# Performance work log

Hardware: AMD Instinct MI355X
Metric: run time of the kernel (lower is better)

Reference implementation:

```python
import jax, jax.numpy as jnp
import numpy as np

TEMPERATURE = 0.07
MARGIN = 0.2
SHUF_ID_OFFSET = 100000


def _normalize(x):
    # matches F.normalize(x + 1e-8, dim=-1) with default eps=1e-12
    v = x + 1e-8
    n = jnp.linalg.norm(v, axis=-1, keepdims=True)
    return v / jnp.maximum(n, 1e-12)


def setup_inputs() -> dict:
    key = jax.random.key(0)
    k1, k2, k3, k4 = jax.random.split(key, 4)
    M, C, D = 1024, 3, 512
    return {
        "motion_embs": jax.random.normal(k1, (M, D), dtype=jnp.float32),
        "text_embs": jax.random.normal(k2, (M, C, D), dtype=jnp.float32),
        "shuffled_text_embs": jax.random.normal(k3, (M, C, D), dtype=jnp.float32),
        "motion_ids": jax.random.randint(k4, (M,), 0, 256, dtype=jnp.int64 if jax.config.jax_enable_x64 else jnp.int32),
    }


def reference(motion_embs, text_embs, shuffled_text_embs, motion_ids):
    M, C, D = text_embs.shape
    m = _normalize(motion_embs)                       # [M, D]
    t = _normalize(text_embs).reshape(M * C, D)       # [M*C, D]
    s = _normalize(shuffled_text_embs).reshape(M * C, D)

    emb = jnp.concatenate([m, t, s], axis=0)          # [N, D], N = M + 2*M*C
    ids = jnp.concatenate([
        motion_ids,
        jnp.repeat(motion_ids, C),
        jnp.repeat(motion_ids + SHUF_ID_OFFSET, C),
    ])

    sim = (emb @ emb.T) / TEMPERATURE                 # [N, N]
    N = emb.shape[0]
    same = ids[None, :] == ids[:, None]
    eye = jnp.eye(N, dtype=bool)
    pos_mask = same & ~eye
    neg_mask = (~same) & ~eye

    exp_sim = jnp.exp(sim)
    # denominator over positives + negatives (all off-diagonal), as in the original
    denom = jnp.sum(jnp.where(pos_mask | neg_mask, exp_sim, 0.0), axis=1)   # [N]
    n_pos = jnp.sum(pos_mask, axis=1)
    n_neg = jnp.sum(neg_mask, axis=1)

    pos_sum = jnp.sum(jnp.where(pos_mask, sim, 0.0), axis=1)
    infonce = jnp.log(denom) - pos_sum / jnp.maximum(n_pos, 1)               # [N]

    margin = jnp.sum(jnp.where(neg_mask, jnp.maximum(sim + MARGIN, 0.0), 0.0), axis=1) / jnp.maximum(n_neg, 1)

    valid = (n_pos > 0) & (n_neg > 0)
    count = jnp.sum(valid)
    total = jnp.sum(jnp.where(valid, infonce + margin, 0.0))
    loss = jnp.where(count > 0, total / jnp.maximum(count, 1), 0.0)
    return loss
```

## Files before the change

### kernel.cpp

```cpp
#include <hip/hip_runtime.h>

#define M_ROWS 1024
#define DIM 512
#define NB 1024
#define N_TOT 7168
#define TEXT_OFF 1024
#define SHUF_OFF 4096
#define INV_T (1.0f/0.07f)
#define MARGIN_V 0.2f
#define TILES 56
#define NBLK 1596
#define SLOT 768

typedef __attribute__((ext_vector_type(8))) short bf16x8;
typedef __attribute__((ext_vector_type(4))) float f32x4;

typedef const __attribute__((address_space(1))) unsigned int gas_uint;
typedef __attribute__((address_space(3))) unsigned int las_uint;

__device__ __forceinline__ void gload16(const void* g, void* l) {
  __builtin_amdgcn_global_load_lds((gas_uint*)g, (las_uint*)l, 16, 0, 0);
}

__device__ __forceinline__ ushort f2bf(float f) {
  unsigned u = __float_as_uint(f);
  u += 0x7fffu + ((u >> 16) & 1u);
  return (ushort)(u >> 16);
}

__device__ __forceinline__ float dpp_sum16(float x) {
  float s = x;
  s += __int_as_float(__builtin_amdgcn_update_dpp(0, __float_as_int(s), 0x111, 0xF, 0xF, true));
  s += __int_as_float(__builtin_amdgcn_update_dpp(0, __float_as_int(s), 0x112, 0xF, 0xF, true));
  s += __int_as_float(__builtin_amdgcn_update_dpp(0, __float_as_int(s), 0x114, 0xF, 0xF, true));
  s += __int_as_float(__builtin_amdgcn_update_dpp(0, __float_as_int(s), 0x118, 0xF, 0xF, true));
  return s;
}

__global__ __launch_bounds__(256) void k_normalize(
    const float* __restrict__ motion, const float* __restrict__ text,
    const float* __restrict__ shuf, const int* __restrict__ mids,
    ushort* __restrict__ emb, int* __restrict__ ids, int* __restrict__ ticket) {
  if (blockIdx.x == 0 && threadIdx.x == 0) *ticket = 0;
  int wave = threadIdx.x >> 6;
  int lane = threadIdx.x & 63;
  int row = blockIdx.x * 4 + wave;
  if (row >= N_TOT) return;
  const float* src;
  int id;
  if (row < TEXT_OFF) { src = motion + (size_t)row * DIM; id = mids[row]; }
  else if (row < SHUF_OFF) { int r = row - TEXT_OFF; src = text + (size_t)r * DIM; id = mids[r / 3]; }
  else { int r = row - SHUF_OFF; src = shuf + (size_t)r * DIM; id = mids[r / 3] + 100000; }

  float4 a = ((const float4*)src)[lane * 2];
  float4 b = ((const float4*)src)[lane * 2 + 1];
  float v0 = a.x + 1e-8f, v1 = a.y + 1e-8f, v2 = a.z + 1e-8f, v3 = a.w + 1e-8f;
  float v4 = b.x + 1e-8f, v5 = b.y + 1e-8f, v6 = b.z + 1e-8f, v7 = b.w + 1e-8f;
  float ss = v0*v0 + v1*v1 + v2*v2 + v3*v3 + v4*v4 + v5*v5 + v6*v6 + v7*v7;
  #pragma unroll
  for (int m = 1; m < 64; m <<= 1) ss += __shfl_xor(ss, m);
  float inv = 1.0f / fmaxf(sqrtf(ss), 1e-12f);

  uint w0 = (uint)f2bf(v0 * inv) | ((uint)f2bf(v1 * inv) << 16);
  uint w1 = (uint)f2bf(v2 * inv) | ((uint)f2bf(v3 * inv) << 16);
  uint w2 = (uint)f2bf(v4 * inv) | ((uint)f2bf(v5 * inv) << 16);
  uint w3 = (uint)f2bf(v6 * inv) | ((uint)f2bf(v7 * inv) << 16);
  uint4 pk; pk.x = w0; pk.y = w1; pk.z = w2; pk.w = w3;
  *((uint4*)(emb + (size_t)row * DIM + lane * 8)) = pk;
  if (lane == 0) ids[row] = id;
}

__global__ __launch_bounds__(256, 3) void k_gemm_loss(
    const ushort* __restrict__ emb, const int* __restrict__ ids,
    float* __restrict__ part) {
  __shared__ ushort Asm[3][4096];
  __shared__ ushort Bsm[3][4096];

  int orig = blockIdx.x;
  int xcd = orig & 7;
  int idx = orig >> 3;
  int bid = (xcd < 4 ? xcd * 200 : 800 + (xcd - 4) * 199) + idx;

  int x = 0;
  while (bid >= TILES - x) { bid -= TILES - x; x++; }
  int y = x + bid;
  bool diag = (x == y);
  int brow = x * 128, bcol = y * 128;
  int tbid = x * TILES - x * (x - 1) / 2 + (y - x);

  int t = threadIdx.x;
  int l = t & 63;
  int w = t >> 6;
  int wr = w >> 1;
  int wc = w & 1;
  int fr = l & 15;
  int fg = l >> 4;

  int srow = w * 16 + (l >> 2);
  int scol = ((l & 3) ^ ((l >> 3) & 3)) * 16;
  const char* gA = (const char*)emb + (size_t)(brow + srow) * NB + scol;
  const char* gB = (const char*)emb + (size_t)(bcol + srow) * NB + scol;
  int ldso = w * 512;

  f32x4 acc[4][4];
  #pragma unroll
  for (int m = 0; m < 4; m++)
    #pragma unroll
    for (int n = 0; n < 4; n++)
      acc[m][n] = (f32x4){0.f, 0.f, 0.f, 0.f};

  int swz = (fg ^ ((fr >> 1) & 3)) * 8;

#define STAGE(T) do { \
    const int _b = (T) % 3; const int _kb = (T) * 64; \
    gload16(gA + _kb,         &Asm[_b][ldso]); \
    gload16(gA + 65536 + _kb, &Asm[_b][2048 + ldso]); \
    gload16(gB + _kb,         &Bsm[_b][ldso]); \
    gload16(gB + 65536 + _kb, &Bsm[_b][2048 + ldso]); \
  } while (0)

  STAGE(0);
  STAGE(1);
  asm volatile("s_waitcnt vmcnt(4)" ::: "memory");
  __builtin_amdgcn_s_barrier();

  #pragma unroll
  for (int tt = 0; tt < 16; tt++) {
    if (tt + 2 < 16) STAGE(tt + 2);
    const int _b = tt % 3;
    const ushort* Ab = &Asm[_b][(wr * 64 + fr) * 32 + swz];
    const ushort* Bb = &Bsm[_b][(wc * 64 + fr) * 32 + swz];
    bf16x8 aF[4], bF[4];
    #pragma unroll
    for (int m = 0; m < 4; m++) aF[m] = *(const bf16x8*)(Ab + m * 512);
    #pragma unroll
    for (int n = 0; n < 4; n++) bF[n] = *(const bf16x8*)(Bb + n * 512);
    __builtin_amdgcn_s_setprio(1);
    #pragma unroll
    for (int m = 0; m < 4; m++)
      #pragma unroll
      for (int n = 0; n < 4; n++)
        acc[m][n] = __builtin_amdgcn_mfma_f32_16x16x32_bf16(aF[m], bF[n], acc[m][n], 0, 0, 0);
    __builtin_amdgcn_s_setprio(0);
    if (tt < 14) {
      asm volatile("s_waitcnt vmcnt(4)" ::: "memory");
      __builtin_amdgcn_s_barrier();
    } else if (tt == 14) {
      asm volatile("s_waitcnt vmcnt(0)" ::: "memory");
      __builtin_amdgcn_s_barrier();
    }
  }
#undef STAGE

  __syncthreads();
  float* rpd = (float*)&Asm[1][0];
  float* rpp = rpd + 256;
  float* rpm = rpp + 256;
  float* cps = (float*)&Bsm[1][0];
  int* ridL = (int*)&Asm[2][0];
  int* cidL = ridL + 128;
  if (t < 128) ridL[t] = ids[brow + t];
  else cidL[t - 128] = ids[bcol + (t - 128)];
  __syncthreads();

  float* ps = part + (size_t)tbid * SLOT;

  int cl = fr;
  int cgrp = fg;
  int cidv[4];
  #pragma unroll
  for (int n = 0; n < 4; n++) cidv[n] = cidL[wc * 64 + n * 16 + cl];
  float cd[4], cp[4], cm[4];
  #pragma unroll
  for (int n = 0; n < 4; n++) { cd[n] = 0.f; cp[n] = 0.f; cm[n] = 0.f; }

  #pragma unroll
  for (int m = 0; m < 4; m++) {
    #pragma unroll
    for (int r = 0; r < 4; r++) {
      int row_l = wr * 64 + m * 16 + cgrp * 4 + r;
      int i = brow + row_l;
      int idi = ridL[row_l];
      float dsum = 0.f, psum = 0.f, msum = 0.f;
      #pragma unroll
      for (int n = 0; n < 4; n++) {
        int col_l = wc * 64 + n * 16 + cl;
        int j = bcol + col_l;
        float sim = acc[m][n][r] * INV_T;
        bool live = (!diag) || (i != j);
        if (live) {
          float e = __expf(sim);
          float hinge = fmaxf(sim + MARGIN_V, 0.f);
          bool same = (idi == cidv[n]);
          float psv = same ? sim : 0.f;
          float msv = same ? 0.f : hinge;
          dsum += e; psum += psv; msum += msv;
          if (!diag) { cd[n] += e; cp[n] += psv; cm[n] += msv; }
        }
      }
      dsum = dpp_sum16(dsum);
      psum = dpp_sum16(psum);
      msum = dpp_sum16(msum);
      if (cl == 15) {
        int o = w * 64 + (row_l & 63);
        rpd[o] = dsum; rpp[o] = psum; rpm[o] = msum;
      }
    }
  }

  if (!diag) {
    #pragma unroll
    for (int n = 0; n < 4; n++) {
      float d = cd[n], p = cp[n], mm = cm[n];
      d += __shfl_xor(d, 16); d += __shfl_xor(d, 32);
      p += __shfl_xor(p, 16); p += __shfl_xor(p, 32);
      mm += __shfl_xor(mm, 16); mm += __shfl_xor(mm, 32);
      if (l < 16) {
        int o = ((w * 4 + n) * 16 + cl) * 3;
        cps[o] = d; cps[o + 1] = p; cps[o + 2] = mm;
      }
    }
  }
  __syncthreads();

  if (t < 128) {
    int b0 = (t >> 6) * 128 + (t & 63);
    float d = rpd[b0] + rpd[b0 + 64];
    float p = rpp[b0] + rpp[b0 + 64];
    float mm = rpm[b0] + rpm[b0 + 64];
    ps[t] = d; ps[128 + t] = p; ps[256 + t] = mm;
  }
  if (!diag && wr == 0 && l < 16) {
    #pragma unroll
    for (int n = 0; n < 4; n++) {
      int o0 = ((w * 4 + n) * 16 + cl) * 3;
      int o1 = (((w + 2) * 4 + n) * 16 + cl) * 3;
      int col_l = w * 64 + n * 16 + cl;
      ps[384 + col_l] = cps[o0] + cps[o1];
      ps[384 + 128 + col_l] = cps[o0 + 1] + cps[o1 + 1];
      ps[384 + 256 + col_l] = cps[o0 + 2] + cps[o1 + 2];
    }
  }
}

__global__ __launch_bounds__(128) void k_reduce(
    const float* __restrict__ part, const int* __restrict__ mids,
    float* __restrict__ blockout, int* __restrict__ ticket,
    float* __restrict__ out) {
  __shared__ int hist[256];
  __shared__ float reds[128];
  __shared__ int redc[128];
  __shared__ int lastf;
  int t = threadIdx.x;
  hist[t] = 0; hist[t + 128] = 0;
  __syncthreads();
  for (int i = t; i < M_ROWS; i += 128) atomicAdd(&hist[mids[i]], 1);
  __syncthreads();

  int p = blockIdx.x;
  int i = p * 128 + t;
  float d = 0.f, pp = 0.f, mm = 0.f;
  int base = p * TILES - p * (p - 1) / 2;
  for (int yy = p; yy < TILES; yy++) {
    const float* s = part + (size_t)(base + yy - p) * SLOT;
    d += s[t]; pp += s[128 + t]; mm += s[256 + t];
  }
  for (int xx = 0; xx < p; xx++) {
    int b = xx * TILES - xx * (xx - 1) / 2 + (p - xx);
    const float* s = part + (size_t)b * SLOT + 384;
    d += s[t]; pp += s[128 + t]; mm += s[256 + t];
  }

  int vmid; bool sh = false;
  if (i < TEXT_OFF) vmid = mids[i];
  else if (i < SHUF_OFF) vmid = mids[(i - TEXT_OFF) / 3];
  else { vmid = mids[(i - SHUF_OFF) / 3]; sh = true; }
  int c = hist[vmid];
  int npos = sh ? (3 * c - 1) : (4 * c - 1);
  int nneg = N_TOT - 1 - npos;
  float val = 0.f; int cnt = 0;
  if (npos > 0 && nneg > 0) {
    val = logf(d) - pp / (float)(npos > 1 ? npos : 1) + mm / (float)(nneg > 1 ? nneg : 1);
    cnt = 1;
  }
  reds[t] = val; redc[t] = cnt;
  __syncthreads();
  for (int s2 = 64; s2 > 0; s2 >>= 1) {
    if (t < s2) { reds[t] += reds[t + s2]; redc[t] += redc[t + s2]; }
    __syncthreads();
  }
  if (t == 0) {
    blockout[p * 2] = reds[0];
    blockout[p * 2 + 1] = (float)redc[0];
    __threadfence();
    int old = atomicAdd(ticket, 1);
    lastf = (old == TILES - 1);
  }
  __syncthreads();
  if (lastf) {
    __threadfence();
    float s = (t < TILES) ? blockout[t * 2] : 0.f;
    float cc = (t < TILES) ? blockout[t * 2 + 1] : 0.f;
    reds[t] = s; redc[t] = (int)cc;
    __syncthreads();
    for (int s2 = 64; s2 > 0; s2 >>= 1) {
      if (t < s2) { reds[t] += reds[t + s2]; redc[t] += redc[t + s2]; }
      __syncthreads();
    }
    if (t == 0) out[0] = (redc[0] > 0) ? reds[0] / (float)redc[0] : 0.f;
  }
}

extern "C" void kernel_launch(void* const* d_in, const int* in_sizes, int n_in,
                              void* d_out, int out_size, void* d_ws, size_t ws_size,
                              hipStream_t stream) {
  const float* motion = (const float*)d_in[0];
  const float* text   = (const float*)d_in[1];
  const float* shuf   = (const float*)d_in[2];
  const int*   mids   = (const int*)d_in[3];

  char* ws = (char*)d_ws;
  ushort* emb = (ushort*)ws;
  int* ids    = (int*)(ws + 7340032);
  float* blockout = (float*)(ws + 7368704);
  int* ticket = (int*)(ws + 7369216);
  float* part = (float*)(ws + 7372800);

  k_normalize<<<N_TOT / 4, 256, 0, stream>>>(motion, text, shuf, mids, emb, ids, ticket);
  k_gemm_loss<<<NBLK, 256, 0, stream>>>(emb, ids, part);
  k_reduce<<<TILES, 128, 0, stream>>>(part, mids, blockout, ticket, (float*)d_out);
}
```

Measured before the change: 81.14 us.

## Give each wave private LDS tiles and split final reduction into separate kernel

Each wave in the GEMM now loads its own 64-row A and B slices into private double-buffered LDS. This removes all block-level barriers from the K loop, at the cost of loading shared rows twice per block, more LDS per block and a lower occupancy hint (2 blocks instead of 3). The loss reduction uses 256-thread blocks, and the atomic-ticket last-block pattern is replaced by a separate single-wave final kernel. That adds one more launch but no longer needs to zero the ticket.

```diff
diff --git a/kernel.cpp b/kernel.cpp
--- a/kernel.cpp
+++ b/kernel.cpp
@@ -40,8 +40,7 @@
 __global__ __launch_bounds__(256) void k_normalize(
     const float* __restrict__ motion, const float* __restrict__ text,
     const float* __restrict__ shuf, const int* __restrict__ mids,
-    ushort* __restrict__ emb, int* __restrict__ ids, int* __restrict__ ticket) {
-  if (blockIdx.x == 0 && threadIdx.x == 0) *ticket = 0;
+    ushort* __restrict__ emb, int* __restrict__ ids) {
   int wave = threadIdx.x >> 6;
   int lane = threadIdx.x & 63;
   int row = blockIdx.x * 4 + wave;
@@ -70,11 +69,11 @@
   if (lane == 0) ids[row] = id;
 }
 
-__global__ __launch_bounds__(256, 3) void k_gemm_loss(
+__global__ __launch_bounds__(256, 2) void k_gemm_loss(
     const ushort* __restrict__ emb, const int* __restrict__ ids,
     float* __restrict__ part) {
-  __shared__ ushort Asm[3][4096];
-  __shared__ ushort Bsm[3][4096];
+  __shared__ ushort Aw[4][2][2048];
+  __shared__ ushort Bw[4][2][2048];
 
   int orig = blockIdx.x;
   int xcd = orig & 7;
@@ -96,11 +95,10 @@
   int fr = l & 15;
   int fg = l >> 4;
 
-  int srow = w * 16 + (l >> 2);
+  int srow = l >> 2;
   int scol = ((l & 3) ^ ((l >> 3) & 3)) * 16;
-  const char* gA = (const char*)emb + (size_t)(brow + srow) * NB + scol;
-  const char* gB = (const char*)emb + (size_t)(bcol + srow) * NB + scol;
-  int ldso = w * 512;
+  const char* gA = (const char*)emb + (size_t)(brow + wr * 64 + srow) * NB + scol;
+  const char* gB = (const char*)emb + (size_t)(bcol + wc * 64 + srow) * NB + scol;
 
   f32x4 acc[4][4];
   #pragma unroll
@@ -112,24 +110,23 @@
   int swz = (fg ^ ((fr >> 1) & 3)) * 8;
 
 #define STAGE(T) do { \
-    const int _b = (T) % 3; const int _kb = (T) * 64; \
-    gload16(gA + _kb,         &Asm[_b][ldso]); \
-    gload16(gA + 65536 + _kb, &Asm[_b][2048 + ldso]); \
-    gload16(gB + _kb,         &Bsm[_b][ldso]); \
-    gload16(gB + 65536 + _kb, &Bsm[_b][2048 + ldso]); \
+    const int _b = (T) & 1; const int _kb = (T) * 64; \
+    _Pragma("unroll") \
+    for (int _g = 0; _g < 4; _g++) { \
+      gload16(gA + (size_t)_g * 16 * NB + _kb, &Aw[w][_b][_g * 512]); \
+      gload16(gB + (size_t)_g * 16 * NB + _kb, &Bw[w][_b][_g * 512]); \
+    } \
   } while (0)
 
   STAGE(0);
-  STAGE(1);
-  asm volatile("s_waitcnt vmcnt(4)" ::: "memory");
-  __builtin_amdgcn_s_barrier();
+  asm volatile("s_waitcnt vmcnt(0)" ::: "memory");
 
   #pragma unroll
   for (int tt = 0; tt < 16; tt++) {
-    if (tt + 2 < 16) STAGE(tt + 2);
-    const int _b = tt % 3;
-    const ushort* Ab = &Asm[_b][(wr * 64 + fr) * 32 + swz];
-    const ushort* Bb = &Bsm[_b][(wc * 64 + fr) * 32 + swz];
+    if (tt < 15) STAGE(tt + 1);
+    const int _b = tt & 1;
+    const ushort* Ab = &Aw[w][_b][fr * 32 + swz];
+    const ushort* Bb = &Bw[w][_b][fr * 32 + swz];
     bf16x8 aF[4], bF[4];
     #pragma unroll
     for (int m = 0; m < 4; m++) aF[m] = *(const bf16x8*)(Ab + m * 512);
@@ -142,25 +139,20 @@
       for (int n = 0; n < 4; n++)
         acc[m][n] = __builtin_amdgcn_mfma_f32_16x16x32_bf16(aF[m], bF[n], acc[m][n], 0, 0, 0);
     __builtin_amdgcn_s_setprio(0);
-    if (tt < 14) {
-      asm volatile("s_waitcnt vmcnt(4)" ::: "memory");
-      __builtin_amdgcn_s_barrier();
-    } else if (tt == 14) {
+    if (tt < 15)
       asm volatile("s_waitcnt vmcnt(0)" ::: "memory");
-      __builtin_amdgcn_s_barrier();
-    }
   }
 #undef STAGE
 
   __syncthreads();
-  float* rpd = (float*)&Asm[1][0];
+  float* rpd = (float*)&Aw[0][0][0];
   float* rpp = rpd + 256;
   float* rpm = rpp + 256;
-  float* cps = (float*)&Bsm[1][0];
-  int* ridL = (int*)&Asm[2][0];
+  float* cps = (float*)&Bw[0][0][0];
+  int* ridL = (int*)&Aw[1][0][0];
   int* cidL = ridL + 128;
   if (t < 128) ridL[t] = ids[brow + t];
-  else cidL[t - 128] = ids[bcol + (t - 128)];
+  else if (t < 256) cidL[t - 128] = ids[bcol + (t - 128)];
   __syncthreads();
 
   float* ps = part + (size_t)tbid * SLOT;
@@ -243,32 +235,31 @@
   }
 }
 
-__global__ __launch_bounds__(128) void k_reduce(
+__global__ __launch_bounds__(256) void k_reduce(
     const float* __restrict__ part, const int* __restrict__ mids,
-    float* __restrict__ blockout, int* __restrict__ ticket,
-    float* __restrict__ out) {
+    float* __restrict__ blockout) {
   __shared__ int hist[256];
-  __shared__ float reds[128];
-  __shared__ int redc[128];
-  __shared__ int lastf;
+  __shared__ float reds[256];
+  __shared__ int redc[256];
   int t = threadIdx.x;
-  hist[t] = 0; hist[t + 128] = 0;
-  __syncthreads();
-  for (int i = t; i < M_ROWS; i += 128) atomicAdd(&hist[mids[i]], 1);
-  __syncthreads();
-
-  int p = blockIdx.x;
-  int i = p * 128 + t;
+  hist[t] = 0;
+  __syncthreads();
+  for (int i = t; i < M_ROWS; i += 256) atomicAdd(&hist[mids[i]], 1);
+  __syncthreads();
+
+  int i = blockIdx.x * 256 + t;
+  int p = i >> 7;
+  int v = i & 127;
   float d = 0.f, pp = 0.f, mm = 0.f;
   int base = p * TILES - p * (p - 1) / 2;
   for (int yy = p; yy < TILES; yy++) {
     const float* s = part + (size_t)(base + yy - p) * SLOT;
-    d += s[t]; pp += s[128 + t]; mm += s[256 + t];
+    d += s[v]; pp += s[128 + v]; mm += s[256 + v];
   }
   for (int xx = 0; xx < p; xx++) {
     int b = xx * TILES - xx * (xx - 1) / 2 + (p - xx);
     const float* s = part + (size_t)b * SLOT + 384;
-    d += s[t]; pp += s[128 + t]; mm += s[256 + t];
+    d += s[v]; pp += s[128 + v]; mm += s[256 + v];
   }
 
   int vmid; bool sh = false;
@@ -285,30 +276,21 @@
   }
   reds[t] = val; redc[t] = cnt;
   __syncthreads();
-  for (int s2 = 64; s2 > 0; s2 >>= 1) {
+  for (int s2 = 128; s2 > 0; s2 >>= 1) {
     if (t < s2) { reds[t] += reds[t + s2]; redc[t] += redc[t + s2]; }
     __syncthreads();
   }
-  if (t == 0) {
-    blockout[p * 2] = reds[0];
-    blockout[p * 2 + 1] = (float)redc[0];
-    __threadfence();
-    int old = atomicAdd(ticket, 1);
-    lastf = (old == TILES - 1);
-  }
-  __syncthreads();
-  if (lastf) {
-    __threadfence();
-    float s = (t < TILES) ? blockout[t * 2] : 0.f;
-    float cc = (t < TILES) ? blockout[t * 2 + 1] : 0.f;
-    reds[t] = s; redc[t] = (int)cc;
-    __syncthreads();
-    for (int s2 = 64; s2 > 0; s2 >>= 1) {
-      if (t < s2) { reds[t] += reds[t + s2]; redc[t] += redc[t + s2]; }
-      __syncthreads();
-    }
-    if (t == 0) out[0] = (redc[0] > 0) ? reds[0] / (float)redc[0] : 0.f;
-  }
+  if (t == 0) { blockout[blockIdx.x * 2] = reds[0]; blockout[blockIdx.x * 2 + 1] = (float)redc[0]; }
+}
+
+__global__ __launch_bounds__(64) void k_final(
+    const float* __restrict__ blockout, float* __restrict__ out) {
+  int t = threadIdx.x;
+  float s = 0.f, c = 0.f;
+  if (t < 28) { s = blockout[t * 2]; c = blockout[t * 2 + 1]; }
+  #pragma unroll
+  for (int m = 32; m > 0; m >>= 1) { s += __shfl_down(s, m); c += __shfl_down(c, m); }
+  if (t == 0) out[0] = (c > 0.f) ? s / c : 0.f;
 }
 
 extern "C" void kernel_launch(void* const* d_in, const int* in_sizes, int n_in,
@@ -323,10 +305,10 @@
   ushort* emb = (ushort*)ws;
   int* ids    = (int*)(ws + 7340032);
   float* blockout = (float*)(ws + 7368704);
-  int* ticket = (int*)(ws + 7369216);
   float* part = (float*)(ws + 7372800);
 
-  k_normalize<<<N_TOT / 4, 256, 0, stream>>>(motion, text, shuf, mids, emb, ids, ticket);
+  k_normalize<<<N_TOT / 4, 256, 0, stream>>>(motion, text, shuf, mids, emb, ids);
   k_gemm_loss<<<NBLK, 256, 0, stream>>>(emb, ids, part);
-  k_reduce<<<TILES, 128, 0, stream>>>(part, mids, blockout, ticket, (float*)d_out);
-}
+  k_reduce<<<TILES / 2, 256, 0, stream>>>(part, mids, blockout);
+  k_final<<<1, 64, 0, stream>>>(blockout, (float*)d_out);
+}
```

Measured after the change: 97.77 us. 1.2x slower.
